# Kernel tuning notes

Measured on AMD Instinct MI355X. Metric: run time of the kernel, lower is better.

## Reference

```python
import jax, jax.numpy as jnp
import numpy as np

N = 20000
E = 320000
IN_C = 256
HID = 64
OUT_C = 64
NUM_LAYERS = 3
HEADS = 8


def setup_inputs() -> dict:
    key = jax.random.key(0)
    ks = jax.random.split(key, 12)
    s_in = 1.0 / np.sqrt(IN_C)
    s_h = 1.0 / np.sqrt(HID)
    inp = {
        "x": jax.random.normal(ks[0], (N, IN_C), dtype=jnp.float32),
        "edge_index": jax.random.randint(ks[1], (2, E), 0, N, dtype=jnp.int64),
        "lin1_w": jax.random.uniform(ks[2], (IN_C, HID), jnp.float32, -s_in, s_in),
        "lin1_b": jnp.zeros((HID,), jnp.float32),
        "wq": jax.random.uniform(ks[3], (NUM_LAYERS, HID, HID), jnp.float32, -s_h, s_h),
        "bq": jnp.zeros((NUM_LAYERS, HID), jnp.float32),
        "wk": jax.random.uniform(ks[4], (NUM_LAYERS, HID, HID), jnp.float32, -s_h, s_h),
        "bk": jnp.zeros((NUM_LAYERS, HID), jnp.float32),
        "wv": jax.random.uniform(ks[5], (NUM_LAYERS, HID, HID), jnp.float32, -s_h, s_h),
        "bv": jnp.zeros((NUM_LAYERS, HID), jnp.float32),
        "lin2_w": jax.random.uniform(ks[6], (HID, OUT_C), jnp.float32, -s_h, s_h),
        "lin2_b": jnp.zeros((OUT_C,), jnp.float32),
    }
    return inp


def reference(x, edge_index, lin1_w, lin1_b, wq, bq, wk, bk, wv, bv, lin2_w, lin2_b):
    n = x.shape[0]
    C = lin1_w.shape[1]
    d = C // HEADS  # per-head dim
    inv_sqrt_d = 1.0 / (d ** 0.5)

    # gcn_norm with self-loops (symmetric normalization, edge weights = 1)
    loop = jnp.arange(n, dtype=edge_index.dtype)
    row = jnp.concatenate([edge_index[0], loop])  # source j
    col = jnp.concatenate([edge_index[1], loop])  # target i
    deg = jax.ops.segment_sum(jnp.ones_like(col, dtype=x.dtype), col, num_segments=n)
    dinv = jnp.where(deg > 0, deg ** -0.5, 0.0)
    norm = dinv[row] * dinv[col]  # [E+N]

    # input projection (dropout inactive in eval mode)
    h = jax.nn.relu(x @ lin1_w + lin1_b)
    x_all = h[:, None, :]  # [N, 1, C] growing history

    for l in range(NUM_LAYERS):
        t = x_all.shape[1]
        # node-level projections (linear commutes with gather)
        q = x_all[:, -1] @ wq[l] + bq[l]                      # [N, C]
        k = jnp.einsum("ntc,cd->ntd", x_all, wk[l]) + bk[l]   # [N, t, C]
        v = jnp.einsum("ntc,cd->ntd", x_all, wv[l]) + bv[l]   # [N, t, C]
        # per-edge multi-head attention of target's latest repr over source history
        Qe = q[col].reshape(-1, HEADS, d)                      # [E', H, d]
        Ke = k[row].reshape(-1, t, HEADS, d)                   # [E', t, H, d]
        Ve = v[row].reshape(-1, t, HEADS, d)
        scores = jnp.einsum("ehd,ethd->eht", Qe, Ke) * inv_sqrt_d
        attn = jax.nn.softmax(scores, axis=-1)                 # [E', H, t]
        msg = jnp.einsum("eht,ethd->ehd", attn, Ve).reshape(-1, C)
        msg = msg * norm[:, None]
        out = jax.ops.segment_sum(msg, col, num_segments=n)    # sum aggregation
        out = jax.nn.relu(out)
        x_all = jnp.concatenate([x_all, out[:, None, :]], axis=1)

    logits = x_all[:, -1] @ lin2_w + lin2_b
    return jax.nn.log_softmax(logits, axis=1)
```

## Files before the change

### kernel.cpp

```cpp
#include <hip/hip_runtime.h>
#include <math.h>

#define HID 64
#define HEADS 8
#define ALD 72

typedef __attribute__((ext_vector_type(8))) short bf16x8;
typedef __attribute__((ext_vector_type(4))) float f32x4;

__device__ __forceinline__ unsigned short f2bf(float f) {
    union { float f; unsigned int u; } cv; cv.f = f;
    unsigned int u = cv.u;
    unsigned int r = (u + 0x7FFFu + ((u >> 16) & 1u)) >> 16;
    return (unsigned short)r;
}
__device__ __forceinline__ float bflo(unsigned int u) {
    union { unsigned int u; float f; } cv; cv.u = u << 16; return cv.f;
}
__device__ __forceinline__ float bfhi(unsigned int u) {
    union { unsigned int u; float f; } cv; cv.u = u & 0xFFFF0000u; return cv.f;
}
__device__ __forceinline__ unsigned relu_pk(unsigned u) {
    unsigned m = ((u & 0x8000u) ? 0u : 0xFFFFu) |
                 ((u & 0x80000000u) ? 0u : 0xFFFF0000u);
    return u & m;
}

__global__ void k_count(const int* __restrict__ col, int* __restrict__ counts, int E) {
    int e = blockIdx.x * blockDim.x + threadIdx.x;
    if (e < E) atomicAdd(&counts[col[e]], 1);
}

__global__ __launch_bounds__(1024) void k_scan(const int* __restrict__ counts,
                                               int* __restrict__ start,
                                               float* __restrict__ dinv, int n) {
    __shared__ int wsum[16];
    int tid = threadIdx.x;
    int lane = tid & 63, wvi = tid >> 6;
    int ipt = (n + 1023) >> 10;
    int c0 = tid * ipt;
    int c1 = min(n, c0 + ipt);
    int s = 0;
    for (int i = c0; i < c1; ++i) s += counts[i];
    int x = s;
#pragma unroll
    for (int off = 1; off < 64; off <<= 1) {
        int y = __shfl_up(x, off);
        if (lane >= off) x += y;
    }
    if (lane == 63) wsum[wvi] = x;
    __syncthreads();
    if (wvi == 0 && lane < 16) {
        int t2 = wsum[lane];
#pragma unroll
        for (int off = 1; off < 16; off <<= 1) {
            int y = __shfl_up(t2, off);
            if (lane >= off) t2 += y;
        }
        wsum[lane] = t2;
    }
    __syncthreads();
    int waveoff = (wvi > 0) ? wsum[wvi - 1] : 0;
    int run = waveoff + x - s;
    for (int i = c0; i < c1; ++i) {
        int v = counts[i];
        start[i] = run;
        dinv[i] = rsqrtf((float)(v + 1));
        run += v;
    }
    if (tid == 0) start[n] = wsum[15];
}

__global__ void k_scatter(const int* __restrict__ ei, const int* __restrict__ start,
                          int* __restrict__ counts, unsigned short* __restrict__ ebuf,
                          int E) {
    int e = blockIdx.x * blockDim.x + threadIdx.x;
    if (e >= E) return;
    int r = ei[e], c = ei[E + e];
    int pos = start[c] + atomicSub(&counts[c], 1) - 1;
    ebuf[pos] = (unsigned short)r;
}

__device__ __forceinline__ void stage_w_bf16(unsigned short* Wt,
                                             const float* __restrict__ w, int tid) {
    for (int idx = tid; idx < 1024; idx += 256) {
        int k = idx >> 4, n4 = (idx & 15) * 4;
        float4 wv = *(const float4*)&w[k * 64 + n4];
        Wt[(n4 + 0) * ALD + k] = f2bf(wv.x);
        Wt[(n4 + 1) * ALD + k] = f2bf(wv.y);
        Wt[(n4 + 2) * ALD + k] = f2bf(wv.z);
        Wt[(n4 + 3) * ALD + k] = f2bf(wv.w);
    }
}

__device__ __forceinline__ void mfma_step(const unsigned short* Alds,
                                          const unsigned short* Wt,
                                          int tid, f32x4 acc[4]) {
    int lane = tid & 63;
    int m0 = (tid >> 6) * 16;
    int c16 = lane & 15, quad = lane >> 4;
    const unsigned short* ar = &Alds[(m0 + c16) * ALD + quad * 8];
    bf16x8 a0 = *(const bf16x8*)ar;
    bf16x8 a1 = *(const bf16x8*)(ar + 32);
#pragma unroll
    for (int nt = 0; nt < 4; ++nt) {
        const unsigned short* br = &Wt[(nt * 16 + c16) * ALD + quad * 8];
        bf16x8 b0 = *(const bf16x8*)br;
        bf16x8 b1 = *(const bf16x8*)(br + 32);
        acc[nt] = __builtin_amdgcn_mfma_f32_16x16x32_bf16(a0, b0, acc[nt], 0, 0, 0);
        acc[nt] = __builtin_amdgcn_mfma_f32_16x16x32_bf16(a1, b1, acc[nt], 0, 0, 0);
    }
}

__global__ __launch_bounds__(256, 4) void k_lin1(
    const float* __restrict__ x, const float* __restrict__ w,
    const float* __restrict__ b, const float* __restrict__ wv0,
    const float* __restrict__ bv0, unsigned short* __restrict__ h,
    unsigned short* __restrict__ kv, int n) {
    __shared__ __align__(16) unsigned short Alds[64 * ALD];
    __shared__ __align__(16) unsigned short Wt[64 * ALD];
    int tid = threadIdx.x;
    int node0 = blockIdx.x * 64;
    f32x4 acc[4];
#pragma unroll
    for (int nt = 0; nt < 4; ++nt) acc[nt] = (f32x4){0.f, 0.f, 0.f, 0.f};

    for (int kc = 0; kc < 256; kc += 64) {
        __syncthreads();
        stage_w_bf16(Wt, w + kc * 64, tid);
        for (int idx = tid; idx < 1024; idx += 256) {
            int r = idx >> 4, c4 = (idx & 15) * 4;
            int node = node0 + r;
            float4 v = make_float4(0.f, 0.f, 0.f, 0.f);
            if (node < n) v = *(const float4*)&x[(size_t)node * 256 + kc + c4];
            Alds[r * ALD + c4 + 0] = f2bf(v.x);
            Alds[r * ALD + c4 + 1] = f2bf(v.y);
            Alds[r * ALD + c4 + 2] = f2bf(v.z);
            Alds[r * ALD + c4 + 3] = f2bf(v.w);
        }
        __syncthreads();
        mfma_step(Alds, Wt, tid, acc);
    }
    int lane = tid & 63;
    int m0 = (tid >> 6) * 16, c16 = lane & 15, quad = lane >> 4;
    float bias[4];
#pragma unroll
    for (int nt = 0; nt < 4; ++nt) bias[nt] = b[nt * 16 + c16];

    __syncthreads();
    stage_w_bf16(Wt, wv0, tid);
#pragma unroll
    for (int i = 0; i < 4; ++i) {
        int row = m0 + quad * 4 + i;
        int node = node0 + row;
#pragma unroll
        for (int nt = 0; nt < 4; ++nt) {
            unsigned short hb = f2bf(fmaxf(acc[nt][i] + bias[nt], 0.f));
            Alds[row * ALD + nt * 16 + c16] = hb;
            if (node < n) h[(size_t)node * 64 + nt * 16 + c16] = hb;
        }
    }
    __syncthreads();
    f32x4 acc2[4];
#pragma unroll
    for (int nt = 0; nt < 4; ++nt) acc2[nt] = (f32x4){0.f, 0.f, 0.f, 0.f};
    mfma_step(Alds, Wt, tid, acc2);
    float bias2[4];
#pragma unroll
    for (int nt = 0; nt < 4; ++nt) bias2[nt] = bv0[nt * 16 + c16];
#pragma unroll
    for (int i = 0; i < 4; ++i) {
        int node = node0 + m0 + quad * 4 + i;
        if (node < n) {
#pragma unroll
            for (int nt = 0; nt < 4; ++nt)
                kv[(size_t)node * 64 + nt * 16 + c16] = f2bf(acc2[nt][i] + bias2[nt]);
        }
    }
}

__global__ __launch_bounds__(256, 4) void k_stage(
    const unsigned short* __restrict__ xs, size_t sstride,
    const float* __restrict__ wk, const float* __restrict__ bk,
    const float* __restrict__ wv, const float* __restrict__ bv,
    unsigned short* __restrict__ kv1, unsigned short* __restrict__ kv2,
    int n, int phase) {
    int j = blockIdx.y;
    int layer, s, isV;
    if (phase == 0) { layer = 1 + (j >> 2); s = j & 1; isV = (j >> 1) & 1; }
    else            { layer = 2; s = 2; isV = j; }
    const unsigned short* src = xs + (size_t)s * sstride;
    const float* w = (isV ? wv : wk) + layer * 4096;
    const float* b = (isV ? bv : bk) + layer * 64;
    unsigned short* dst = (layer == 1) ? kv1 : kv2;
    int stride = (layer == 1) ? 256 : 384;
    int koff = s * 128 + (isV ? 64 : 0);
    bool relu_in = (s >= 1);

    __shared__ __align__(16) unsigned short Alds[64 * ALD];
    __shared__ __align__(16) unsigned short Wt[64 * ALD];
    int tid = threadIdx.x;
    int node0 = blockIdx.x * 64;
    stage_w_bf16(Wt, w, tid);
    for (int idx = tid; idx < 512; idx += 256) {
        int r = idx >> 3, seg = idx & 7;
        int node = node0 + r;
        uint4 u = make_uint4(0u, 0u, 0u, 0u);
        if (node < n) u = *(const uint4*)&src[(size_t)node * 64 + seg * 8];
        if (relu_in) {
            u.x = relu_pk(u.x); u.y = relu_pk(u.y);
            u.z = relu_pk(u.z); u.w = relu_pk(u.w);
        }
        *(uint4*)&Alds[r * ALD + seg * 8] = u;
    }
    __syncthreads();
    f32x4 acc[4];
#pragma unroll
    for (int nt = 0; nt < 4; ++nt) acc[nt] = (f32x4){0.f, 0.f, 0.f, 0.f};
    mfma_step(Alds, Wt, tid, acc);

    int lane = tid & 63;
    int m0 = (tid >> 6) * 16, c16 = lane & 15, quad = lane >> 4;
    float bias[4];
#pragma unroll
    for (int nt = 0; nt < 4; ++nt) bias[nt] = b[nt * 16 + c16];
#pragma unroll
    for (int i = 0; i < 4; ++i) {
        int node = node0 + m0 + quad * 4 + i;
        if (node < n) {
#pragma unroll
            for (int nt = 0; nt < 4; ++nt)
                dst[(size_t)node * stride + koff + nt * 16 + c16] =
                    f2bf(acc[nt][i] + bias[nt]);
        }
    }
}

template <int T, bool FINAL>
__global__ __launch_bounds__(256) void k_attn(
    const int* __restrict__ start, const unsigned short* __restrict__ ebuf,
    const float* __restrict__ dinv, const unsigned short* __restrict__ xs,
    size_t sstride, const unsigned short* __restrict__ kv,
    const float* __restrict__ wq, const float* __restrict__ bq,
    const float* __restrict__ w2, const float* __restrict__ b2,
    unsigned short* __restrict__ outb, float* __restrict__ outf, int n) {
    const int KVS = (T == 1) ? 64 : T * 128;
    int node = (int)((blockIdx.x * (size_t)blockDim.x + threadIdx.x) >> 6);
    int lane = threadIdx.x & 63;
    if (node >= n) return;
    int g = lane >> 3;
    int cb = (lane & 7) * 8;

    float qv[8];
    if (T > 1) {
        const float isd = 0.35355339059327373f;
        uint4 xu = *(const uint4*)&xs[(size_t)(T - 1) * sstride +
                                      (size_t)node * 64 + cb];
        float xq[8] = {fmaxf(bflo(xu.x), 0.f), fmaxf(bfhi(xu.x), 0.f),
                       fmaxf(bflo(xu.y), 0.f), fmaxf(bfhi(xu.y), 0.f),
                       fmaxf(bflo(xu.z), 0.f), fmaxf(bfhi(xu.z), 0.f),
                       fmaxf(bflo(xu.w), 0.f), fmaxf(bfhi(xu.w), 0.f)};
        float qo = bq[lane];
#pragma unroll
        for (int c = 0; c < 64; ++c)
            qo += __shfl(xq[c & 7], c >> 3) * wq[c * 64 + lane];
#pragma unroll
        for (int d = 0; d < 8; ++d) qv[d] = __shfl(qo, (lane & 7) * 8 + d) * isd;
    }

    float dc = dinv[node];
    int s0 = start[node];
    int cnt = start[node + 1] - s0 + 1;

    float acc[8];
#pragma unroll
    for (int k = 0; k < 8; ++k) acc[k] = 0.f;

    int nch = (cnt + 7) >> 3;
    int idx = g;
    bool v_cur = idx < cnt;
    int r_cur = node;
    if (v_cur && idx > 0) r_cur = ebuf[s0 + idx - 1];

    for (int c = 0; c < nch; ++c) {
        int idxn = idx + 8;
        bool v_nxt = idxn < cnt;
        int r_nxt = node;
        if (v_nxt) r_nxt = ebuf[s0 + idxn - 1];

        float dr = v_cur ? dinv[r_cur] : 0.f;
        const unsigned short* rkv = kv + (size_t)r_cur * KVS;

        float sc[T];
        float wgt;
        if (T > 1) {
            float m = -1e30f;
#pragma unroll
            for (int s = 0; s < T; ++s) {
                uint4 ku = *(const uint4*)&rkv[s * 128 + cb];
                float p = qv[0] * bflo(ku.x) + qv[1] * bfhi(ku.x)
                        + qv[2] * bflo(ku.y) + qv[3] * bfhi(ku.y)
                        + qv[4] * bflo(ku.z) + qv[5] * bfhi(ku.z)
                        + qv[6] * bflo(ku.w) + qv[7] * bfhi(ku.w);
                sc[s] = p;
                m = fmaxf(m, p);
            }
            float denom = 0.f;
#pragma unroll
            for (int s = 0; s < T; ++s) { sc[s] = __expf(sc[s] - m); denom += sc[s]; }
            wgt = dr / denom;
        } else {
            sc[0] = 1.f;
            wgt = dr;
        }

        float mg[8];
#pragma unroll
        for (int k = 0; k < 8; ++k) mg[k] = 0.f;
#pragma unroll
        for (int s = 0; s < T; ++s) {
            uint4 vu = *(const uint4*)&rkv[((T == 1) ? 0 : s * 128 + 64) + cb];
            float wv_ = sc[s];
            mg[0] += wv_ * bflo(vu.x); mg[1] += wv_ * bfhi(vu.x);
            mg[2] += wv_ * bflo(vu.y); mg[3] += wv_ * bfhi(vu.y);
            mg[4] += wv_ * bflo(vu.z); mg[5] += wv_ * bfhi(vu.z);
            mg[6] += wv_ * bflo(vu.w); mg[7] += wv_ * bfhi(vu.w);
        }
#pragma unroll
        for (int k = 0; k < 8; ++k) acc[k] += wgt * mg[k];

        r_cur = r_nxt; v_cur = v_nxt; idx = idxn;
    }

#pragma unroll
    for (int off = 8; off < 64; off <<= 1) {
#pragma unroll
        for (int k = 0; k < 8; ++k) acc[k] += __shfl_xor(acc[k], off);
    }

    if (!FINAL) {
        if (g == 0) {
            ushort4 o0, o1;
            o0.x = f2bf(acc[0] * dc); o0.y = f2bf(acc[1] * dc);
            o0.z = f2bf(acc[2] * dc); o0.w = f2bf(acc[3] * dc);
            o1.x = f2bf(acc[4] * dc); o1.y = f2bf(acc[5] * dc);
            o1.z = f2bf(acc[6] * dc); o1.w = f2bf(acc[7] * dc);
            *(ushort4*)&outb[(size_t)node * 64 + cb] = o0;
            *(ushort4*)&outb[(size_t)node * 64 + cb + 4] = o1;
        }
    } else {
        float lg = b2[lane];
#pragma unroll
        for (int c = 0; c < 64; ++c) {
            float xc = fmaxf(__shfl(acc[c & 7], c >> 3) * dc, 0.f);
            lg += xc * w2[c * 64 + lane];
        }
        float mx = lg;
#pragma unroll
        for (int off = 1; off < 64; off <<= 1) mx = fmaxf(mx, __shfl_xor(mx, off));
        float e = __expf(lg - mx);
        float ssum = e;
#pragma unroll
        for (int off = 1; off < 64; off <<= 1) ssum += __shfl_xor(ssum, off);
        outf[(size_t)node * 64 + lane] = lg - mx - __logf(ssum);
    }
}

extern "C" void kernel_launch(void* const* d_in, const int* in_sizes, int n_in,
                              void* d_out, int out_size, void* d_ws, size_t ws_size,
                              hipStream_t stream) {
    const float* x  = (const float*)d_in[0];
    const int*   ei = (const int*)d_in[1];
    const float* w1 = (const float*)d_in[2];
    const float* b1 = (const float*)d_in[3];
    const float* wq = (const float*)d_in[4];
    const float* bq = (const float*)d_in[5];
    const float* wk = (const float*)d_in[6];
    const float* bk = (const float*)d_in[7];
    const float* wv = (const float*)d_in[8];
    const float* bv = (const float*)d_in[9];
    const float* w2 = (const float*)d_in[10];
    const float* b2 = (const float*)d_in[11];
    float* outp = (float*)d_out;

    int n = in_sizes[0] / 256;
    int E = in_sizes[1] / 2;

    float* ws = (float*)d_ws;
    size_t off = 0;
    float* dinv = ws + off; off += (size_t)n;
    unsigned short* xsU = (unsigned short*)(ws + off); off += (size_t)n * 96;
    unsigned short* kv0 = (unsigned short*)(ws + off); off += (size_t)n * 32;
    unsigned short* kv1 = (unsigned short*)(ws + off); off += (size_t)n * 128;
    unsigned short* kv2 = (unsigned short*)(ws + off); off += (size_t)n * 192;
    int* wsI    = (int*)(ws + off);
    int* counts = wsI;
    int* startA = wsI + n;
    unsigned short* ebuf = (unsigned short*)(wsI + 2 * n + 1);

    size_t sstride = (size_t)n * 64;

    hipMemsetAsync(counts, 0, (size_t)n * sizeof(int), stream);
    k_count<<<(E + 255) / 256, 256, 0, stream>>>(ei + E, counts, E);
    k_scan<<<1, 1024, 0, stream>>>(counts, startA, dinv, n);
    k_scatter<<<(E + 255) / 256, 256, 0, stream>>>(ei, startA, counts, ebuf, E);

    k_lin1<<<(n + 63) / 64, 256, 0, stream>>>(x, w1, b1, wv, bv, xsU, kv0, n);

    int attn_grid = (int)(((size_t)n * 64 + 255) / 256);
    int NT = (n + 63) / 64;

    k_attn<1, false><<<attn_grid, 256, 0, stream>>>(
        startA, ebuf, dinv, xsU, sstride, kv0, nullptr, nullptr, nullptr, nullptr,
        xsU + sstride, nullptr, n);

    {
        dim3 grid(NT, 8);
        k_stage<<<grid, 256, 0, stream>>>(xsU, sstride, wk, bk, wv, bv,
                                          kv1, kv2, n, 0);
    }
    k_attn<2, false><<<attn_grid, 256, 0, stream>>>(
        startA, ebuf, dinv, xsU, sstride, kv1, wq + 4096, bq + 64, nullptr, nullptr,
        xsU + 2 * sstride, nullptr, n);

    {
        dim3 grid(NT, 2);
        k_stage<<<grid, 256, 0, stream>>>(xsU, sstride, wk, bk, wv, bv,
                                          kv1, kv2, n, 1);
    }
    k_attn<3, true><<<attn_grid, 256, 0, stream>>>(
        startA, ebuf, dinv, xsU, sstride, kv2, wq + 8192, bq + 128, w2, b2,
        nullptr, outp, n);
}
```

Before: 285.7 us.

## Prefetch next edge K/V rows in attention loop and rebalance stage launches

The attention edge loop now loads the next neighbor's K/V vectors and dinv one iteration ahead, so gather latency overlaps with the current edge's softmax and accumulate. The Q projection is rewritten to read the node's full row directly instead of broadcasting through cross-lane shuffles. The layer-2 K/V projections for history slots 0 and 1 move from the first stage launch to the second, which shortens the first launch and lengthens the second. The prefetch adds register pressure and an extra row gather at the end of each node's edge list.

```diff
diff --git a/kernel.cpp b/kernel.cpp
--- a/kernel.cpp
+++ b/kernel.cpp
@@ -24,6 +24,18 @@
     unsigned m = ((u & 0x8000u) ? 0u : 0xFFFFu) |
                  ((u & 0x80000000u) ? 0u : 0xFFFF0000u);
     return u & m;
+}
+
+__device__ __forceinline__ float dot8(const float* qp, uint4 u) {
+    return qp[0] * bflo(u.x) + qp[1] * bfhi(u.x) + qp[2] * bflo(u.y) +
+           qp[3] * bfhi(u.y) + qp[4] * bflo(u.z) + qp[5] * bfhi(u.z) +
+           qp[6] * bflo(u.w) + qp[7] * bfhi(u.w);
+}
+__device__ __forceinline__ void axpy8(float a, uint4 u, float* Y) {
+    Y[0] += a * bflo(u.x); Y[1] += a * bfhi(u.x);
+    Y[2] += a * bflo(u.y); Y[3] += a * bfhi(u.y);
+    Y[4] += a * bflo(u.z); Y[5] += a * bfhi(u.z);
+    Y[6] += a * bflo(u.w); Y[7] += a * bfhi(u.w);
 }
 
 __global__ void k_count(const int* __restrict__ col, int* __restrict__ counts, int E) {
@@ -187,8 +199,8 @@
     int n, int phase) {
     int j = blockIdx.y;
     int layer, s, isV;
-    if (phase == 0) { layer = 1 + (j >> 2); s = j & 1; isV = (j >> 1) & 1; }
-    else            { layer = 2; s = 2; isV = j; }
+    if (phase == 0) { layer = 1; s = j & 1; isV = j >> 1; }
+    else            { layer = 2; s = j >> 1; isV = j & 1; }
     const unsigned short* src = xs + (size_t)s * sstride;
     const float* w = (isV ? wv : wk) + layer * 4096;
     const float* b = (isV ? bv : bk) + layer * 64;
@@ -254,18 +266,26 @@
     float qv[8];
     if (T > 1) {
         const float isd = 0.35355339059327373f;
-        uint4 xu = *(const uint4*)&xs[(size_t)(T - 1) * sstride +
-                                      (size_t)node * 64 + cb];
-        float xq[8] = {fmaxf(bflo(xu.x), 0.f), fmaxf(bfhi(xu.x), 0.f),
-                       fmaxf(bflo(xu.y), 0.f), fmaxf(bfhi(xu.y), 0.f),
-                       fmaxf(bflo(xu.z), 0.f), fmaxf(bfhi(xu.z), 0.f),
-                       fmaxf(bflo(xu.w), 0.f), fmaxf(bfhi(xu.w), 0.f)};
-        float qo = bq[lane];
-#pragma unroll
-        for (int c = 0; c < 64; ++c)
-            qo += __shfl(xq[c & 7], c >> 3) * wq[c * 64 + lane];
-#pragma unroll
-        for (int d = 0; d < 8; ++d) qv[d] = __shfl(qo, (lane & 7) * 8 + d) * isd;
+        const unsigned short* xrow =
+            &xs[(size_t)(T - 1) * sstride + (size_t)node * 64];
+        float a0 = 0.f, a1 = 0.f, a2 = 0.f, a3 = 0.f;
+        float a4 = 0.f, a5 = 0.f, a6 = 0.f, a7 = 0.f;
+#pragma unroll
+        for (int w8 = 0; w8 < 8; ++w8) {
+            uint4 u = *(const uint4*)&xrow[w8 * 8];
+            const float* wc = &wq[(w8 * 8) * 64 + lane];
+            a0 += fmaxf(bflo(u.x), 0.f) * wc[0 * 64];
+            a1 += fmaxf(bfhi(u.x), 0.f) * wc[1 * 64];
+            a2 += fmaxf(bflo(u.y), 0.f) * wc[2 * 64];
+            a3 += fmaxf(bfhi(u.y), 0.f) * wc[3 * 64];
+            a4 += fmaxf(bflo(u.z), 0.f) * wc[4 * 64];
+            a5 += fmaxf(bfhi(u.z), 0.f) * wc[5 * 64];
+            a6 += fmaxf(bflo(u.w), 0.f) * wc[6 * 64];
+            a7 += fmaxf(bfhi(u.w), 0.f) * wc[7 * 64];
+        }
+        float qo = bq[lane] + (((a0 + a1) + (a2 + a3)) + ((a4 + a5) + (a6 + a7)));
+#pragma unroll
+        for (int d = 0; d < 8; ++d) qv[d] = __shfl(qo, cb + d) * isd;
     }
 
     float dc = dinv[node];
@@ -278,58 +298,71 @@
 
     int nch = (cnt + 7) >> 3;
     int idx = g;
-    bool v_cur = idx < cnt;
-    int r_cur = node;
-    if (v_cur && idx > 0) r_cur = ebuf[s0 + idx - 1];
-
-    for (int c = 0; c < nch; ++c) {
-        int idxn = idx + 8;
-        bool v_nxt = idxn < cnt;
-        int r_nxt = node;
-        if (v_nxt) r_nxt = ebuf[s0 + idxn - 1];
-
-        float dr = v_cur ? dinv[r_cur] : 0.f;
-        const unsigned short* rkv = kv + (size_t)r_cur * KVS;
-
-        float sc[T];
-        float wgt;
-        if (T > 1) {
-            float m = -1e30f;
+    bool vc = idx < cnt;
+    int rc = node;
+    if (vc && idx > 0) rc = ebuf[s0 + idx - 1];
+    float drc = vc ? dinv[rc] : 0.f;
+    {
+        const unsigned short* pc = kv + (size_t)rc * KVS;
+        uint4 Kc[T], Vc[T];
+#pragma unroll
+        for (int s = 0; s < T; ++s) {
+            if (T > 1) Kc[s] = *(const uint4*)&pc[s * 128 + cb];
+            Vc[s] = *(const uint4*)&pc[((T == 1) ? 0 : s * 128 + 64) + cb];
+        }
+
+        for (int c = 0; c < nch; ++c) {
+            int idxn = idx + 8;
+            bool vn = idxn < cnt;
+            int rn = node;
+            if (vn) rn = ebuf[s0 + idxn - 1];
+            float drn = vn ? dinv[rn] : 0.f;
+            const unsigned short* pn = kv + (size_t)rn * KVS;
+            uint4 Kn[T], Vn[T];
 #pragma unroll
             for (int s = 0; s < T; ++s) {
-                uint4 ku = *(const uint4*)&rkv[s * 128 + cb];
-                float p = qv[0] * bflo(ku.x) + qv[1] * bfhi(ku.x)
-                        + qv[2] * bflo(ku.y) + qv[3] * bfhi(ku.y)
-                        + qv[4] * bflo(ku.z) + qv[5] * bfhi(ku.z)
-                        + qv[6] * bflo(ku.w) + qv[7] * bfhi(ku.w);
-                sc[s] = p;
-                m = fmaxf(m, p);
+                if (T > 1) Kn[s] = *(const uint4*)&pn[s * 128 + cb];
+                Vn[s] = *(const uint4*)&pn[((T == 1) ? 0 : s * 128 + 64) + cb];
             }
-            float denom = 0.f;
-#pragma unroll
-            for (int s = 0; s < T; ++s) { sc[s] = __expf(sc[s] - m); denom += sc[s]; }
-            wgt = dr / denom;
-        } else {
-            sc[0] = 1.f;
-            wgt = dr;
-        }
-
-        float mg[8];
-#pragma unroll
-        for (int k = 0; k < 8; ++k) mg[k] = 0.f;
-#pragma unroll
-        for (int s = 0; s < T; ++s) {
-            uint4 vu = *(const uint4*)&rkv[((T == 1) ? 0 : s * 128 + 64) + cb];
-            float wv_ = sc[s];
-            mg[0] += wv_ * bflo(vu.x); mg[1] += wv_ * bfhi(vu.x);
-            mg[2] += wv_ * bflo(vu.y); mg[3] += wv_ * bfhi(vu.y);
-            mg[4] += wv_ * bflo(vu.z); mg[5] += wv_ * bfhi(vu.z);
-            mg[6] += wv_ * bflo(vu.w); mg[7] += wv_ * bfhi(vu.w);
-        }
-#pragma unroll
-        for (int k = 0; k < 8; ++k) acc[k] += wgt * mg[k];
-
-        r_cur = r_nxt; v_cur = v_nxt; idx = idxn;
+
+            float sc[T];
+            float wgt;
+            if (T > 1) {
+                float m = -1e30f;
+#pragma unroll
+                for (int s = 0; s < T; ++s) {
+                    float p = dot8(qv, Kc[s]);
+                    sc[s] = p;
+                    m = fmaxf(m, p);
+                }
+                float denom = 0.f;
+#pragma unroll
+                for (int s = 0; s < T; ++s) {
+                    sc[s] = __expf(sc[s] - m);
+                    denom += sc[s];
+                }
+                wgt = drc / denom;
+            } else {
+                sc[0] = 1.f;
+                wgt = drc;
+            }
+
+            float mg[8];
+#pragma unroll
+            for (int k = 0; k < 8; ++k) mg[k] = 0.f;
+#pragma unroll
+            for (int s = 0; s < T; ++s) axpy8(sc[s], Vc[s], mg);
+#pragma unroll
+            for (int k = 0; k < 8; ++k) acc[k] += wgt * mg[k];
+
+#pragma unroll
+            for (int s = 0; s < T; ++s) {
+                if (T > 1) Kc[s] = Kn[s];
+                Vc[s] = Vn[s];
+            }
+            drc = drn;
+            idx = idxn;
+        }
     }
 
 #pragma unroll
@@ -415,7 +448,7 @@
         xsU + sstride, nullptr, n);
 
     {
-        dim3 grid(NT, 8);
+        dim3 grid(NT, 4);
         k_stage<<<grid, 256, 0, stream>>>(xsU, sstride, wk, bk, wv, bv,
                                           kv1, kv2, n, 0);
     }
@@ -424,7 +457,7 @@
         xsU + 2 * sstride, nullptr, n);
 
     {
-        dim3 grid(NT, 2);
+        dim3 grid(NT, 6);
         k_stage<<<grid, 256, 0, stream>>>(xsU, sstride, wk, bk, wv, bv,
                                           kv1, kv2, n, 1);
     }
```

Result: faster. 269.5 us (-5.7%).

## Fuse scan into lin1, scatter into stage, precompute Q via MFMA, use dot2 bf16

Applied to the files above, without the earlier changes.

The single-block scan now runs as an extra block of the lin1 kernel, and the edge scatter is merged with the layer-1/2 K/V projections of history slot 0 into one launch, removing two launches and their serialization. The per-node query projection moves out of the attention kernel's shuffle-based matvec into the MFMA stage kernel, which writes an fp32 Q buffer. Attention scores now use packed v_dot2_f32_bf16 on a bf16-rounded query, which adds rounding error. The edge-prefetch software pipeline is removed in favour of a simpler loop, and the extra fp32 Q buffer adds memory traffic.

```diff
diff --git a/kernel.cpp b/kernel.cpp
--- a/kernel.cpp
+++ b/kernel.cpp
@@ -26,20 +26,26 @@
     return u & m;
 }
 
+__device__ __forceinline__ float dot2bf(unsigned a, unsigned b, float c) {
+    float d;
+    asm("v_dot2_f32_bf16 %0, %1, %2, %3" : "=v"(d) : "v"(a), "v"(b), "v"(c));
+    return d;
+}
+
 __global__ void k_count(const int* __restrict__ col, int* __restrict__ counts, int E) {
     int e = blockIdx.x * blockDim.x + threadIdx.x;
     if (e < E) atomicAdd(&counts[col[e]], 1);
 }
 
-__global__ __launch_bounds__(1024) void k_scan(const int* __restrict__ counts,
-                                               int* __restrict__ start,
-                                               float* __restrict__ dinv, int n) {
-    __shared__ int wsum[16];
-    int tid = threadIdx.x;
+__device__ __forceinline__ void scan256_body(const int* __restrict__ counts,
+                                             int* __restrict__ start,
+                                             float* __restrict__ dinv, int n,
+                                             int tid, int* sscan) {
     int lane = tid & 63, wvi = tid >> 6;
-    int ipt = (n + 1023) >> 10;
+    int ipt = (n + 255) >> 8;
     int c0 = tid * ipt;
     int c1 = min(n, c0 + ipt);
+    if (c0 > n) c0 = n;
     int s = 0;
     for (int i = c0; i < c1; ++i) s += counts[i];
     int x = s;
@@ -48,37 +54,22 @@
         int y = __shfl_up(x, off);
         if (lane >= off) x += y;
     }
-    if (lane == 63) wsum[wvi] = x;
+    if (lane == 63) sscan[wvi] = x;
     __syncthreads();
-    if (wvi == 0 && lane < 16) {
-        int t2 = wsum[lane];
-#pragma unroll
-        for (int off = 1; off < 16; off <<= 1) {
-            int y = __shfl_up(t2, off);
-            if (lane >= off) t2 += y;
-        }
-        wsum[lane] = t2;
+    if (tid == 0) {
+        int r = 0;
+#pragma unroll
+        for (int i = 0; i < 4; ++i) { int t = sscan[i]; sscan[i + 4] = r; r += t; }
+        start[n] = r;
     }
     __syncthreads();
-    int waveoff = (wvi > 0) ? wsum[wvi - 1] : 0;
-    int run = waveoff + x - s;
+    int run = sscan[wvi + 4] + (x - s);
     for (int i = c0; i < c1; ++i) {
         int v = counts[i];
         start[i] = run;
         dinv[i] = rsqrtf((float)(v + 1));
         run += v;
     }
-    if (tid == 0) start[n] = wsum[15];
-}
-
-__global__ void k_scatter(const int* __restrict__ ei, const int* __restrict__ start,
-                          int* __restrict__ counts, unsigned short* __restrict__ ebuf,
-                          int E) {
-    int e = blockIdx.x * blockDim.x + threadIdx.x;
-    if (e >= E) return;
-    int r = ei[e], c = ei[E + e];
-    int pos = start[c] + atomicSub(&counts[c], 1) - 1;
-    ebuf[pos] = (unsigned short)r;
 }
 
 __device__ __forceinline__ void stage_w_bf16(unsigned short* Wt,
@@ -112,14 +103,72 @@
     }
 }
 
-__global__ __launch_bounds__(256, 4) void k_lin1(
+__device__ __forceinline__ void stage_tile_body(
+    const unsigned short* __restrict__ src, const float* __restrict__ w,
+    const float* __restrict__ b, float* __restrict__ qd,
+    unsigned short* __restrict__ kvdst, int kv_stride, int kv_off, bool relu_in,
+    int node0, int n, int tid, unsigned short* Alds, unsigned short* Wt) {
+    stage_w_bf16(Wt, w, tid);
+    for (int idx = tid; idx < 512; idx += 256) {
+        int r = idx >> 3, seg = idx & 7;
+        int node = node0 + r;
+        uint4 u = make_uint4(0u, 0u, 0u, 0u);
+        if (node < n) u = *(const uint4*)&src[(size_t)node * 64 + seg * 8];
+        if (relu_in) {
+            u.x = relu_pk(u.x); u.y = relu_pk(u.y);
+            u.z = relu_pk(u.z); u.w = relu_pk(u.w);
+        }
+        *(uint4*)&Alds[r * ALD + seg * 8] = u;
+    }
+    __syncthreads();
+    f32x4 acc[4];
+#pragma unroll
+    for (int nt = 0; nt < 4; ++nt) acc[nt] = (f32x4){0.f, 0.f, 0.f, 0.f};
+    mfma_step(Alds, Wt, tid, acc);
+
+    int lane = tid & 63;
+    int m0 = (tid >> 6) * 16, c16 = lane & 15, quad = lane >> 4;
+    float bias[4];
+#pragma unroll
+    for (int nt = 0; nt < 4; ++nt) bias[nt] = b[nt * 16 + c16];
+    if (qd) {
+#pragma unroll
+        for (int i = 0; i < 4; ++i) {
+            int node = node0 + m0 + quad * 4 + i;
+            if (node < n) {
+#pragma unroll
+                for (int nt = 0; nt < 4; ++nt)
+                    qd[(size_t)node * 64 + nt * 16 + c16] = acc[nt][i] + bias[nt];
+            }
+        }
+    } else {
+#pragma unroll
+        for (int i = 0; i < 4; ++i) {
+            int node = node0 + m0 + quad * 4 + i;
+            if (node < n) {
+#pragma unroll
+                for (int nt = 0; nt < 4; ++nt)
+                    kvdst[(size_t)node * kv_stride + kv_off + nt * 16 + c16] =
+                        f2bf(acc[nt][i] + bias[nt]);
+            }
+        }
+    }
+}
+
+__global__ __launch_bounds__(256, 4) void k_lin1_scan(
     const float* __restrict__ x, const float* __restrict__ w,
     const float* __restrict__ b, const float* __restrict__ wv0,
     const float* __restrict__ bv0, unsigned short* __restrict__ h,
-    unsigned short* __restrict__ kv, int n) {
+    unsigned short* __restrict__ kv, const int* __restrict__ counts,
+    int* __restrict__ startA, float* __restrict__ dinv, int n, int NT) {
     __shared__ __align__(16) unsigned short Alds[64 * ALD];
     __shared__ __align__(16) unsigned short Wt[64 * ALD];
+    __shared__ int sscan[8];
     int tid = threadIdx.x;
+    if (blockIdx.x == (unsigned)NT) {
+        scan256_body(counts, startA, dinv, n, tid, sscan);
+        return;
+    }
     int node0 = blockIdx.x * 64;
     f32x4 acc[4];
 #pragma unroll
@@ -179,69 +228,78 @@
     }
 }
 
-__global__ __launch_bounds__(256, 4) void k_stage(
-    const unsigned short* __restrict__ xs, size_t sstride,
+__global__ __launch_bounds__(256, 4) void k_scatter_stage(
+    const int* __restrict__ ei, const int* __restrict__ startA,
+    int* __restrict__ counts, unsigned short* __restrict__ ebuf, int E, int nsb,
+    const unsigned short* __restrict__ xs,
     const float* __restrict__ wk, const float* __restrict__ bk,
     const float* __restrict__ wv, const float* __restrict__ bv,
     unsigned short* __restrict__ kv1, unsigned short* __restrict__ kv2,
-    int n, int phase) {
-    int j = blockIdx.y;
-    int layer, s, isV;
-    if (phase == 0) { layer = 1 + (j >> 2); s = j & 1; isV = (j >> 1) & 1; }
-    else            { layer = 2; s = 2; isV = j; }
-    const unsigned short* src = xs + (size_t)s * sstride;
+    int n, int NT) {
+    __shared__ __align__(16) unsigned short Alds[64 * ALD];
+    __shared__ __align__(16) unsigned short Wt[64 * ALD];
+    int bx = blockIdx.x;
+    if (bx < nsb) {
+        int e = bx * 256 + threadIdx.x;
+        if (e < E) {
+            int r = ei[e], c = ei[E + e];
+            int pos = startA[c] + atomicSub(&counts[c], 1) - 1;
+            ebuf[pos] = (unsigned short)r;
+        }
+        return;
+    }
+    int t = bx - nsb;
+    int j = t / NT, tile = t - j * NT;
+    int layer = 1 + (j >> 1), isV = j & 1;
     const float* w = (isV ? wv : wk) + layer * 4096;
     const float* b = (isV ? bv : bk) + layer * 64;
     unsigned short* dst = (layer == 1) ? kv1 : kv2;
     int stride = (layer == 1) ? 256 : 384;
-    int koff = s * 128 + (isV ? 64 : 0);
-    bool relu_in = (s >= 1);
-
+    int koff = isV ? 64 : 0;
+    stage_tile_body(xs, w, b, nullptr, dst, stride, koff, false,
+                    tile * 64, n, threadIdx.x, Alds, Wt);
+}
+
+__global__ __launch_bounds__(256, 4) void k_stage(
+    const unsigned short* __restrict__ xs, size_t sstride,
+    const float* __restrict__ wq, const float* __restrict__ bq,
+    const float* __restrict__ wk, const float* __restrict__ bk,
+    const float* __restrict__ wv, const float* __restrict__ bv,
+    float* __restrict__ qbuf, unsigned short* __restrict__ kv1,
+    unsigned short* __restrict__ kv2, int n, int phase) {
     __shared__ __align__(16) unsigned short Alds[64 * ALD];
     __shared__ __align__(16) unsigned short Wt[64 * ALD];
-    int tid = threadIdx.x;
-    int node0 = blockIdx.x * 64;
-    stage_w_bf16(Wt, w, tid);
-    for (int idx = tid; idx < 512; idx += 256) {
-        int r = idx >> 3, seg = idx & 7;
-        int node = node0 + r;
-        uint4 u = make_uint4(0u, 0u, 0u, 0u);
-        if (node < n) u = *(const uint4*)&src[(size_t)node * 64 + seg * 8];
-        if (relu_in) {
-            u.x = relu_pk(u.x); u.y = relu_pk(u.y);
-            u.z = relu_pk(u.z); u.w = relu_pk(u.w);
-        }
-        *(uint4*)&Alds[r * ALD + seg * 8] = u;
-    }
-    __syncthreads();
-    f32x4 acc[4];
-#pragma unroll
-    for (int nt = 0; nt < 4; ++nt) acc[nt] = (f32x4){0.f, 0.f, 0.f, 0.f};
-    mfma_step(Alds, Wt, tid, acc);
-
-    int lane = tid & 63;
-    int m0 = (tid >> 6) * 16, c16 = lane & 15, quad = lane >> 4;
-    float bias[4];
-#pragma unroll
-    for (int nt = 0; nt < 4; ++nt) bias[nt] = b[nt * 16 + c16];
-#pragma unroll
-    for (int i = 0; i < 4; ++i) {
-        int node = node0 + m0 + quad * 4 + i;
-        if (node < n) {
-#pragma unroll
-            for (int nt = 0; nt < 4; ++nt)
-                dst[(size_t)node * stride + koff + nt * 16 + c16] =
-                    f2bf(acc[nt][i] + bias[nt]);
-        }
-    }
+    int j = blockIdx.y;
+    int layer, s, isV = 0, isQ = 0;
+    if (phase == 1) {
+        if (j < 4) { layer = 1 + (j >> 1); isV = j & 1; s = 1; }
+        else       { layer = 1; isQ = 1; s = 1; }
+    } else {
+        if (j < 2) { layer = 2; isV = j; s = 2; }
+        else       { layer = 2; isQ = 1; s = 2; }
+    }
+    const unsigned short* src = xs + (size_t)s * sstride;
+    const float* w; const float* b;
+    float* qd = nullptr; unsigned short* dst = nullptr;
+    int stride = 0, koff = 0;
+    if (isQ) {
+        w = wq + layer * 4096; b = bq + layer * 64; qd = qbuf;
+    } else {
+        w = (isV ? wv : wk) + layer * 4096;
+        b = (isV ? bv : bk) + layer * 64;
+        dst = (layer == 1) ? kv1 : kv2;
+        stride = (layer == 1) ? 256 : 384;
+        koff = s * 128 + (isV ? 64 : 0);
+    }
+    stage_tile_body(src, w, b, qd, dst, stride, koff, true,
+                    blockIdx.x * 64, n, threadIdx.x, Alds, Wt);
 }
 
 template <int T, bool FINAL>
 __global__ __launch_bounds__(256) void k_attn(
     const int* __restrict__ start, const unsigned short* __restrict__ ebuf,
-    const float* __restrict__ dinv, const unsigned short* __restrict__ xs,
-    size_t sstride, const unsigned short* __restrict__ kv,
-    const float* __restrict__ wq, const float* __restrict__ bq,
+    const float* __restrict__ dinv, const float* __restrict__ q,
+    const unsigned short* __restrict__ kv,
     const float* __restrict__ w2, const float* __restrict__ b2,
     unsigned short* __restrict__ outb, float* __restrict__ outf, int n) {
     const int KVS = (T == 1) ? 64 : T * 128;
@@ -251,23 +309,16 @@
     int g = lane >> 3;
     int cb = (lane & 7) * 8;
 
-    float qv[8];
+    unsigned qpk[4];
     if (T > 1) {
         const float isd = 0.35355339059327373f;
-        uint4 xu = *(const uint4*)&xs[(size_t)(T - 1) * sstride +
-                                      (size_t)node * 64 + cb];
-        float xq[8] = {fmaxf(bflo(xu.x), 0.f), fmaxf(bfhi(xu.x), 0.f),
-                       fmaxf(bflo(xu.y), 0.f), fmaxf(bfhi(xu.y), 0.f),
-                       fmaxf(bflo(xu.z), 0.f), fmaxf(bfhi(xu.z), 0.f),
-                       fmaxf(bflo(xu.w), 0.f), fmaxf(bfhi(xu.w), 0.f)};
-        float qo = bq[lane];
-#pragma unroll
-        for (int c = 0; c < 64; ++c)
-            qo += __shfl(xq[c & 7], c >> 3) * wq[c * 64 + lane];
-#pragma unroll
-        for (int d = 0; d < 8; ++d) qv[d] = __shfl(qo, (lane & 7) * 8 + d) * isd;
-    }
-
+        float4 q0 = *(const float4*)&q[(size_t)node * 64 + cb];
+        float4 q1 = *(const float4*)&q[(size_t)node * 64 + cb + 4];
+        qpk[0] = ((unsigned)f2bf(q0.y * isd) << 16) | (unsigned)f2bf(q0.x * isd);
+        qpk[1] = ((unsigned)f2bf(q0.w * isd) << 16) | (unsigned)f2bf(q0.z * isd);
+        qpk[2] = ((unsigned)f2bf(q1.y * isd) << 16) | (unsigned)f2bf(q1.x * isd);
+        qpk[3] = ((unsigned)f2bf(q1.w * isd) << 16) | (unsigned)f2bf(q1.z * isd);
+    }
     float dc = dinv[node];
     int s0 = start[node];
     int cnt = start[node + 1] - s0 + 1;
@@ -276,60 +327,46 @@
 #pragma unroll
     for (int k = 0; k < 8; ++k) acc[k] = 0.f;
 
-    int nch = (cnt + 7) >> 3;
-    int idx = g;
-    bool v_cur = idx < cnt;
-    int r_cur = node;
-    if (v_cur && idx > 0) r_cur = ebuf[s0 + idx - 1];
-
-    for (int c = 0; c < nch; ++c) {
-        int idxn = idx + 8;
-        bool v_nxt = idxn < cnt;
-        int r_nxt = node;
-        if (v_nxt) r_nxt = ebuf[s0 + idxn - 1];
-
-        float dr = v_cur ? dinv[r_cur] : 0.f;
-        const unsigned short* rkv = kv + (size_t)r_cur * KVS;
-
-        float sc[T];
-        float wgt;
+    for (int base = 0; base < cnt; base += 8) {
+        int idx = base + g;
+        bool valid = idx < cnt;
+        int r = node;
+        if (valid && idx > 0) r = ebuf[s0 + idx - 1];
+        float dr = valid ? dinv[r] : 0.f;
+        const unsigned short* rkv = kv + (size_t)r * KVS;
+
+        float cf[T];
         if (T > 1) {
+            float sc[T];
             float m = -1e30f;
 #pragma unroll
             for (int s = 0; s < T; ++s) {
                 uint4 ku = *(const uint4*)&rkv[s * 128 + cb];
-                float p = qv[0] * bflo(ku.x) + qv[1] * bfhi(ku.x)
-                        + qv[2] * bflo(ku.y) + qv[3] * bfhi(ku.y)
-                        + qv[4] * bflo(ku.z) + qv[5] * bfhi(ku.z)
-                        + qv[6] * bflo(ku.w) + qv[7] * bfhi(ku.w);
+                float p = dot2bf(qpk[3], ku.w,
+                          dot2bf(qpk[2], ku.z,
+                          dot2bf(qpk[1], ku.y,
+                          dot2bf(qpk[0], ku.x, 0.f))));
                 sc[s] = p;
                 m = fmaxf(m, p);
             }
             float denom = 0.f;
 #pragma unroll
             for (int s = 0; s < T; ++s) { sc[s] = __expf(sc[s] - m); denom += sc[s]; }
-            wgt = dr / denom;
+            float w = dr / denom;
+#pragma unroll
+            for (int s = 0; s < T; ++s) cf[s] = w * sc[s];
         } else {
-            sc[0] = 1.f;
-            wgt = dr;
-        }
-
-        float mg[8];
-#pragma unroll
-        for (int k = 0; k < 8; ++k) mg[k] = 0.f;
+            cf[0] = dr;
+        }
 #pragma unroll
         for (int s = 0; s < T; ++s) {
             uint4 vu = *(const uint4*)&rkv[((T == 1) ? 0 : s * 128 + 64) + cb];
-            float wv_ = sc[s];
-            mg[0] += wv_ * bflo(vu.x); mg[1] += wv_ * bfhi(vu.x);
-            mg[2] += wv_ * bflo(vu.y); mg[3] += wv_ * bfhi(vu.y);
-            mg[4] += wv_ * bflo(vu.z); mg[5] += wv_ * bfhi(vu.z);
-            mg[6] += wv_ * bflo(vu.w); mg[7] += wv_ * bfhi(vu.w);
-        }
-#pragma unroll
-        for (int k = 0; k < 8; ++k) acc[k] += wgt * mg[k];
-
-        r_cur = r_nxt; v_cur = v_nxt; idx = idxn;
+            float wv_ = cf[s];
+            acc[0] += wv_ * bflo(vu.x); acc[1] += wv_ * bfhi(vu.x);
+            acc[2] += wv_ * bflo(vu.y); acc[3] += wv_ * bfhi(vu.y);
+            acc[4] += wv_ * bflo(vu.z); acc[5] += wv_ * bfhi(vu.z);
+            acc[6] += wv_ * bflo(vu.w); acc[7] += wv_ * bfhi(vu.w);
+        }
     }
 
 #pragma unroll
@@ -389,6 +426,7 @@
     float* ws = (float*)d_ws;
     size_t off = 0;
     float* dinv = ws + off; off += (size_t)n;
+    float* qbuf = ws + off; off += (size_t)n * 64;
     unsigned short* xsU = (unsigned short*)(ws + off); off += (size_t)n * 96;
     unsigned short* kv0 = (unsigned short*)(ws + off); off += (size_t)n * 32;
     unsigned short* kv1 = (unsigned short*)(ws + off); off += (size_t)n * 128;
@@ -399,36 +437,32 @@
     unsigned short* ebuf = (unsigned short*)(wsI + 2 * n + 1);
 
     size_t sstride = (size_t)n * 64;
+    int NT = (n + 63) / 64;
+    int nsb = (E + 255) / 256;
+    int attn_grid = (int)(((size_t)n * 64 + 255) / 256);
 
     hipMemsetAsync(counts, 0, (size_t)n * sizeof(int), stream);
-    k_count<<<(E + 255) / 256, 256, 0, stream>>>(ei + E, counts, E);
-    k_scan<<<1, 1024, 0, stream>>>(counts, startA, dinv, n);
-    k_scatter<<<(E + 255) / 256, 256, 0, stream>>>(ei, startA, counts, ebuf, E);
-
-    k_lin1<<<(n + 63) / 64, 256, 0, stream>>>(x, w1, b1, wv, bv, xsU, kv0, n);
-
-    int attn_grid = (int)(((size_t)n * 64 + 255) / 256);
-    int NT = (n + 63) / 64;
-
+    k_count<<<nsb, 256, 0, stream>>>(ei + E, counts, E);
+    k_lin1_scan<<<NT + 1, 256, 0, stream>>>(x, w1, b1, wv, bv, xsU, kv0,
+                                            counts, startA, dinv, n, NT);
+    k_scatter_stage<<<nsb + 4 * NT, 256, 0, stream>>>(
+        ei, startA, counts, ebuf, E, nsb, xsU, wk, bk, wv, bv, kv1, kv2, n, NT);
     k_attn<1, false><<<attn_grid, 256, 0, stream>>>(
-        startA, ebuf, dinv, xsU, sstride, kv0, nullptr, nullptr, nullptr, nullptr,
+        startA, ebuf, dinv, nullptr, kv0, nullptr, nullptr,
         xsU + sstride, nullptr, n);
-
     {
-        dim3 grid(NT, 8);
-        k_stage<<<grid, 256, 0, stream>>>(xsU, sstride, wk, bk, wv, bv,
-                                          kv1, kv2, n, 0);
+        dim3 grid(NT, 5);
+        k_stage<<<grid, 256, 0, stream>>>(xsU, sstride, wq, bq, wk, bk, wv, bv,
+                                          qbuf, kv1, kv2, n, 1);
     }
     k_attn<2, false><<<attn_grid, 256, 0, stream>>>(
-        startA, ebuf, dinv, xsU, sstride, kv1, wq + 4096, bq + 64, nullptr, nullptr,
+        startA, ebuf, dinv, qbuf, kv1, nullptr, nullptr,
         xsU + 2 * sstride, nullptr, n);
-
     {
-        dim3 grid(NT, 2);
-        k_stage<<<grid, 256, 0, stream>>>(xsU, sstride, wk, bk, wv, bv,
-                                          kv1, kv2, n, 1);
+        dim3 grid(NT, 3);
+        k_stage<<<grid, 256, 0, stream>>>(xsU, sstride, wq, bq, wk, bk, wv, bv,
+                                          qbuf, kv1, kv2, n, 2);
     }
     k_attn<3, true><<<attn_grid, 256, 0, stream>>>(
-        startA, ebuf, dinv, xsU, sstride, kv2, wq + 8192, bq + 128, w2, b2,
-        nullptr, outp, n);
-}
+        startA, ebuf, dinv, qbuf, kv2, w2, b2, nullptr, outp, n);
+}
```

New measurement: 256.6 us. 10.2% less time.
